# Performance work log

Measured on AMD Instinct MI355X. Metric: run time of the kernel, lower is better.

Reference implementation:

```python
import jax, jax.numpy as jnp
import numpy as np

B, S, H = 8, 1024, 1024
NH, HD = 16, 64
LN_EPS = 1e-12


def setup_inputs() -> dict:
    key = jax.random.key(0)
    ks = jax.random.split(key, 8)
    sd = 0.02
    return {
        "hidden_states": jax.random.normal(ks[0], (B, S, H), jnp.float32),
        "attention_mask": jnp.zeros((B, 1, 1, S), jnp.float32),
        "Wq": jax.random.normal(ks[1], (H, H), jnp.float32) * sd,
        "bq": jnp.zeros((H,), jnp.float32),
        "Wk": jax.random.normal(ks[2], (H, H), jnp.float32) * sd,
        "bk": jnp.zeros((H,), jnp.float32),
        "Wv": jax.random.normal(ks[3], (H, H), jnp.float32) * sd,
        "bv": jnp.zeros((H,), jnp.float32),
        "Wo": jax.random.normal(ks[4], (H, H), jnp.float32) * sd,
        "bo": jnp.zeros((H,), jnp.float32),
        "ln_gamma": jnp.ones((H,), jnp.float32),
        "ln_beta": jnp.zeros((H,), jnp.float32),
    }


def _heads(x):
    # [B,S,H] -> [B,NH,S,HD]
    return x.reshape(B, S, NH, HD).transpose(0, 2, 1, 3)


def reference(hidden_states, attention_mask, Wq, bq, Wk, bk, Wv, bv, Wo, bo, ln_gamma, ln_beta):
    # QKV projections (torch Linear: x @ W.T + b)
    q = _heads(hidden_states @ Wq.T + bq)
    k = _heads(hidden_states @ Wk.T + bk)
    v = _heads(hidden_states @ Wv.T + bv)
    # scaled dot-product attention with additive mask
    scores = jnp.einsum("bhqd,bhkd->bhqk", q, k) / np.sqrt(HD).astype(np.float32)
    scores = scores + attention_mask  # broadcast [B,1,1,S]
    probs = jax.nn.softmax(scores, axis=-1)
    ctx = jnp.einsum("bhqk,bhkd->bhqd", probs, v)
    ctx = ctx.transpose(0, 2, 1, 3).reshape(B, S, H)
    # output projection + residual + LayerNorm
    out = ctx @ Wo.T + bo
    x = out + hidden_states
    mu = jnp.mean(x, axis=-1, keepdims=True)
    var = jnp.var(x, axis=-1, keepdims=True)
    return (x - mu) * jax.lax.rsqrt(var + LN_EPS) * ln_gamma + ln_beta
```

## Files before the change

kernel.cpp:

```cpp
#include <hip/hip_runtime.h>
#include <stdint.h>

typedef __attribute__((ext_vector_type(8))) __bf16 bf16x8;
typedef __attribute__((ext_vector_type(8))) unsigned short ushortx8;
typedef __attribute__((ext_vector_type(4))) unsigned short ushortx4;
typedef __attribute__((ext_vector_type(4))) short short4v;
typedef __attribute__((ext_vector_type(4))) float floatx4;

#define LOG2E 1.4426950408889634f
#define QSCALE 0.18033688011112043f

#define ASYNC16(g, l) __builtin_amdgcn_global_load_lds( \
    (__attribute__((address_space(1))) void*)(g),       \
    (__attribute__((address_space(3))) void*)(l), 16, 0, 0)

__device__ __forceinline__ unsigned short f2bf(float f) {
    unsigned int u = __float_as_uint(f);
    u += 0x7fffu + ((u >> 16) & 1u);
    return (unsigned short)(u >> 16);
}

__device__ __forceinline__ floatx4 mfma32(bf16x8 a, bf16x8 b, floatx4 c) {
    return __builtin_amdgcn_mfma_f32_16x16x32_bf16(a, b, c, 0, 0, 0);
}
__device__ __forceinline__ floatx4 mfma16(short4v a, short4v b, floatx4 c) {
    return __builtin_amdgcn_mfma_f32_16x16x16bf16_1k(a, b, c, 0, 0, 0);
}

__global__ __launch_bounds__(256) void cvt_all(
    const float* __restrict__ hidden,
    const float* __restrict__ Wq, const float* __restrict__ Wk,
    const float* __restrict__ Wv, const float* __restrict__ Wo,
    unsigned short* __restrict__ hid_bf,
    unsigned short* __restrict__ oqkv, unsigned short* __restrict__ oo)
{
    const float* src;
    unsigned short* dst;
    int i;
    if (blockIdx.x < 4096) {
        src = hidden; dst = hid_bf;
        i = blockIdx.x * 256 + threadIdx.x;
    } else {
        int blk = (blockIdx.x - 4096) >> 9;
        src = (blk == 0) ? Wq : (blk == 1) ? Wk : (blk == 2) ? Wv : Wo;
        dst = (blk == 3) ? oo : oqkv + (size_t)blk * 1048576;
        i = ((blockIdx.x - 4096) & 511) * 256 + threadIdx.x;
    }
    const float4* p = (const float4*)src + (size_t)i * 2;
    float4 a = p[0], b = p[1];
    ushortx8 o;
    o[0] = f2bf(a.x); o[1] = f2bf(a.y); o[2] = f2bf(a.z); o[3] = f2bf(a.w);
    o[4] = f2bf(b.x); o[5] = f2bf(b.y); o[6] = f2bf(b.z); o[7] = f2bf(b.w);
    *((ushortx8*)dst + i) = o;
}

template<bool SWAP>
__device__ __forceinline__ void kloop_bk64(
    const unsigned short* __restrict__ Ag,
    const unsigned short* __restrict__ Wg,
    unsigned short* As, unsigned short* Bs,
    int wm, int wn, int l16, int quad, int t,
    floatx4 acc[4][4])
{
#pragma unroll 1
    for (int k0 = 0; k0 < 1024; k0 += 64) {
        __syncthreads();
#pragma unroll
        for (int i = 0; i < 4; i++) {
            ASYNC16(Ag + (size_t)i * 32 * 1024 + k0, As + i * 2048 + t * 8);
            ASYNC16(Wg + (size_t)i * 32 * 1024 + k0, Bs + i * 2048 + t * 8);
        }
        __syncthreads();
#pragma unroll
        for (int s = 0; s < 2; s++) {
            int pb = ((s * 4 + quad) ^ (l16 & 7)) * 8;
            bf16x8 af[4], bfr[4];
#pragma unroll
            for (int mt = 0; mt < 4; mt++)
                af[mt] = *(const bf16x8*)(As + (wm + mt * 16 + l16) * 64 + pb);
#pragma unroll
            for (int nt = 0; nt < 4; nt++)
                bfr[nt] = *(const bf16x8*)(Bs + (wn + nt * 16 + l16) * 64 + pb);
            if (SWAP) {
#pragma unroll
                for (int ft = 0; ft < 4; ft++)
#pragma unroll
                    for (int st = 0; st < 4; st++)
                        acc[ft][st] = mfma32(bfr[ft], af[st], acc[ft][st]);
            } else {
#pragma unroll
                for (int mt = 0; mt < 4; mt++)
#pragma unroll
                    for (int nt = 0; nt < 4; nt++)
                        acc[mt][nt] = mfma32(af[mt], bfr[nt], acc[mt][nt]);
            }
        }
    }
}

__global__ __launch_bounds__(256) void gemm_qkv(
    const unsigned short* __restrict__ A,
    const unsigned short* __restrict__ W,
    const float* __restrict__ bq, const float* __restrict__ bk, const float* __restrict__ bv,
    unsigned short* __restrict__ Qo, unsigned short* __restrict__ Ko,
    unsigned short* __restrict__ Vo)
{
    __shared__ unsigned short As[128 * 64];
    __shared__ unsigned short Bs[128 * 64];
    const int t = threadIdx.x;
    const int wave = t >> 6, lane = t & 63;
    const int quad = lane >> 4, l16 = lane & 15;
    const int wm = (wave >> 1) * 64, wn = (wave & 1) * 64;
    const int srow = t >> 3;
    const int scol = ((t & 7) ^ (srow & 7)) * 8;

    const unsigned short* Ag = A + ((size_t)blockIdx.x * 128 + srow) * 1024 + scol;
    const unsigned short* Wg = W + ((size_t)blockIdx.y * 128 + srow) * 1024 + scol;

    floatx4 acc[4][4] = {};
    kloop_bk64<true>(Ag, Wg, As, Bs, wm, wn, l16, quad, t, acc);

    int y = blockIdx.y;
    if (y < 16) {
        const float* bp = (y < 8) ? bq : bk;
        unsigned short* op = (y < 8) ? Qo : Ko;
        float sc = (y < 8) ? QSCALE : 1.0f;
#pragma unroll
        for (int ft = 0; ft < 4; ft++) {
            int featg = (y * 128 + wn + ft * 16 + quad * 4) & 1023;
            float4 b4 = *(const float4*)(bp + featg);
            int h = featg >> 6, d = featg & 63;
#pragma unroll
            for (int st = 0; st < 4; st++) {
                int sg = blockIdx.x * 128 + wm + st * 16 + l16;
                int b = sg >> 10, s = sg & 1023;
                ushortx4 o4;
                o4[0] = f2bf((acc[ft][st][0] + b4.x) * sc);
                o4[1] = f2bf((acc[ft][st][1] + b4.y) * sc);
                o4[2] = f2bf((acc[ft][st][2] + b4.z) * sc);
                o4[3] = f2bf((acc[ft][st][3] + b4.w) * sc);
                *(ushortx4*)(op + (((size_t)(b * 16 + h) * 1024 + s) * 64 + d)) = o4;
            }
        }
    } else {
#pragma unroll
        for (int ft = 0; ft < 4; ft++) {
            int featg = (y * 128 + wn + ft * 16 + quad * 4) & 1023;
            float4 b4 = *(const float4*)(bv + featg);
#pragma unroll
            for (int r = 0; r < 4; r++) {
                int feat = featg + r;
                int h = feat >> 6, d = feat & 63;
                float bias = (r == 0) ? b4.x : (r == 1) ? b4.y : (r == 2) ? b4.z : b4.w;
#pragma unroll
                for (int st = 0; st < 4; st++) {
                    int sg = blockIdx.x * 128 + wm + st * 16 + l16;
                    int b = sg >> 10, s = sg & 1023;
                    int sp = (s & ~63) + (st >> 1) * 32 + (l16 >> 2) * 8 + (st & 1) * 4 + (l16 & 3);
                    Vo[((size_t)(b * 16 + h) * 64 + d) * 1024 + sp] = f2bf(acc[ft][st][r] + bias);
                }
            }
        }
    }
}

__global__ __launch_bounds__(256) void attn(
    const unsigned short* __restrict__ Q,
    const unsigned short* __restrict__ Kg,
    const unsigned short* __restrict__ Vt,
    const float* __restrict__ mask,
    unsigned short* __restrict__ ctx)
{
    __shared__ unsigned short Qs[128 * 64];
    __shared__ unsigned short Ks[64 * 64];
    __shared__ unsigned short Vs[64 * 64];
    __shared__ float Msall[1024];

    const int t = threadIdx.x;
    const int wave = t >> 6, lane = t & 63, quad = lane >> 4, l16 = lane & 15;
    const int s7 = l16 & 7;
    const int head = blockIdx.y;
    const int b = head >> 4, h = head & 15;
    const int q0 = blockIdx.x * 128;
    const unsigned short* Qh = Q + (size_t)head * 65536;
    const unsigned short* Kh = Kg + (size_t)head * 65536;
    const unsigned short* Vh = Vt + (size_t)head * 65536;

    const int srow = t >> 3;
    const int scol = ((t & 7) ^ (srow & 7)) * 8;

    {
        float4 m4 = *(const float4*)(mask + b * 1024 + t * 4);
        m4.x *= LOG2E; m4.y *= LOG2E; m4.z *= LOG2E; m4.w *= LOG2E;
        *(float4*)(Msall + t * 4) = m4;
    }

#pragma unroll
    for (int i = 0; i < 4; i++)
        ASYNC16(Qh + (size_t)(q0 + i * 32 + srow) * 64 + scol, Qs + i * 2048 + t * 8);
    __syncthreads();

    bf16x8 qf[2][2];
#pragma unroll
    for (int qg = 0; qg < 2; qg++) {
        int qrow = wave * 32 + qg * 16 + l16;
#pragma unroll
        for (int s = 0; s < 2; s++)
            qf[qg][s] = *(const bf16x8*)(Qs + qrow * 64 + (((s * 4 + quad) ^ s7) * 8));
    }

    const short4v ones = {(short)0x3F80, (short)0x3F80, (short)0x3F80, (short)0x3F80};
    floatx4 acc_l[2] = {};
    floatx4 o_acc[2][4] = {};

    for (int k0 = 0; k0 < 1024; k0 += 64) {
        __syncthreads();
#pragma unroll
        for (int i = 0; i < 2; i++) {
            ASYNC16(Kh + (size_t)(k0 + i * 32 + srow) * 64 + scol, Ks + i * 2048 + t * 8);
            ASYNC16(Vh + (size_t)(i * 32 + srow) * 1024 + k0 + scol, Vs + i * 2048 + t * 8);
        }
        __syncthreads();

        bf16x8 kf[4][2];
        floatx4 mk[4];
#pragma unroll
        for (int nt = 0; nt < 4; nt++) {
            int krow = nt * 16 + l16;
#pragma unroll
            for (int s = 0; s < 2; s++)
                kf[nt][s] = *(const bf16x8*)(Ks + krow * 64 + (((s * 4 + quad) ^ s7) * 8));
            mk[nt] = *(const floatx4*)(Msall + k0 + nt * 16 + quad * 4);
        }

        short4v pf[2][4];
#pragma unroll
        for (int qg = 0; qg < 2; qg++) {
#pragma unroll
            for (int nt = 0; nt < 4; nt++) {
                floatx4 z = {0.f, 0.f, 0.f, 0.f};
                z = mfma32(kf[nt][0], qf[qg][0], z);
                z = mfma32(kf[nt][1], qf[qg][1], z);
#pragma unroll
                for (int r = 0; r < 4; r++) {
                    float p = exp2f(z[r] + mk[nt][r]);
                    pf[qg][nt][r] = (short)(__float_as_uint(p) >> 16);
                }
            }
        }

#pragma unroll
        for (int nt = 0; nt < 4; nt++) {
            acc_l[0] = mfma16(ones, pf[0][nt], acc_l[0]);
            acc_l[1] = mfma16(ones, pf[1][nt], acc_l[1]);
        }

#pragma unroll
        for (int dt = 0; dt < 4; dt++) {
            int vrow = dt * 16 + l16;
            ushortx8 v01 = *(const ushortx8*)(Vs + vrow * 64 + ((quad ^ s7) * 8));
            ushortx8 v23 = *(const ushortx8*)(Vs + vrow * 64 + (((quad + 4) ^ s7) * 8));
            short4v vf0 = {(short)v01[0], (short)v01[1], (short)v01[2], (short)v01[3]};
            short4v vf1 = {(short)v01[4], (short)v01[5], (short)v01[6], (short)v01[7]};
            short4v vf2 = {(short)v23[0], (short)v23[1], (short)v23[2], (short)v23[3]};
            short4v vf3 = {(short)v23[4], (short)v23[5], (short)v23[6], (short)v23[7]};
#pragma unroll
            for (int qg = 0; qg < 2; qg++) {
                o_acc[qg][dt] = mfma16(vf0, pf[qg][0], o_acc[qg][dt]);
                o_acc[qg][dt] = mfma16(vf1, pf[qg][1], o_acc[qg][dt]);
                o_acc[qg][dt] = mfma16(vf2, pf[qg][2], o_acc[qg][dt]);
                o_acc[qg][dt] = mfma16(vf3, pf[qg][3], o_acc[qg][dt]);
            }
        }
    }

#pragma unroll
    for (int qg = 0; qg < 2; qg++) {
        float inv_l = 1.0f / acc_l[qg][0];
        int qg_row = q0 + wave * 32 + qg * 16 + l16;
#pragma unroll
        for (int dt = 0; dt < 4; dt++) {
            ushortx4 o4;
#pragma unroll
            for (int r = 0; r < 4; r++) o4[r] = f2bf(o_acc[qg][dt][r] * inv_l);
            *(ushortx4*)(ctx + ((size_t)(b * 1024 + qg_row)) * 1024 + h * 64 + dt * 16 + quad * 4) = o4;
        }
    }
}

__global__ __launch_bounds__(256) void gemm_proj(
    const unsigned short* __restrict__ A,
    const unsigned short* __restrict__ W,
    const float* __restrict__ bo,
    const float* __restrict__ resid,
    float* __restrict__ X)
{
    __shared__ unsigned short As[128 * 64];
    __shared__ unsigned short Bs[128 * 64];
    const int t = threadIdx.x;
    const int wave = t >> 6, lane = t & 63;
    const int quad = lane >> 4, l16 = lane & 15;
    const int wm = (wave >> 1) * 64, wn = (wave & 1) * 64;
    const int srow = t >> 3;
    const int scol = ((t & 7) ^ (srow & 7)) * 8;

    const unsigned short* Ag = A + ((size_t)blockIdx.x * 128 + srow) * 1024 + scol;
    const unsigned short* Wg = W + ((size_t)blockIdx.y * 128 + srow) * 1024 + scol;

    floatx4 acc[4][4] = {};
    kloop_bk64<false>(Ag, Wg, As, Bs, wm, wn, l16, quad, t, acc);

#pragma unroll
    for (int nt = 0; nt < 4; nt++) {
        int gn = blockIdx.y * 128 + wn + nt * 16 + l16;
        float bias = bo[gn];
#pragma unroll
        for (int mt = 0; mt < 4; mt++) {
#pragma unroll
            for (int r = 0; r < 4; r++) {
                int gm = blockIdx.x * 128 + wm + mt * 16 + quad * 4 + r;
                size_t off = (size_t)gm * 1024 + gn;
                X[off] = acc[mt][nt][r] + bias + resid[off];
            }
        }
    }
}

__global__ __launch_bounds__(256) void ln_k(const float* __restrict__ X,
                                            const float* __restrict__ g,
                                            const float* __restrict__ be,
                                            float* __restrict__ out)
{
    int row = blockIdx.x;
    int t = threadIdx.x;
    const float* xr = X + (size_t)row * 1024;
    float4 v = *(const float4*)(xr + t * 4);
    float s = v.x + v.y + v.z + v.w;
    float ss = v.x * v.x + v.y * v.y + v.z * v.z + v.w * v.w;
    for (int off = 1; off < 64; off <<= 1) {
        s += __shfl_xor(s, off);
        ss += __shfl_xor(ss, off);
    }
    __shared__ float red[8];
    int wave = t >> 6, lane = t & 63;
    if (lane == 0) { red[wave] = s; red[4 + wave] = ss; }
    __syncthreads();
    s = red[0] + red[1] + red[2] + red[3];
    ss = red[4] + red[5] + red[6] + red[7];
    float mu = s * (1.f / 1024.f);
    float var = ss * (1.f / 1024.f) - mu * mu;
    float inv = rsqrtf(var + 1e-12f);
    float4 gv = *(const float4*)(g + t * 4);
    float4 bv = *(const float4*)(be + t * 4);
    float4 o;
    o.x = (v.x - mu) * inv * gv.x + bv.x;
    o.y = (v.y - mu) * inv * gv.y + bv.y;
    o.z = (v.z - mu) * inv * gv.z + bv.z;
    o.w = (v.w - mu) * inv * gv.w + bv.w;
    *(float4*)(out + (size_t)row * 1024 + t * 4) = o;
}

extern "C" void kernel_launch(void* const* d_in, const int* in_sizes, int n_in,
                              void* d_out, int out_size, void* d_ws, size_t ws_size,
                              hipStream_t stream)
{
    const float* hidden = (const float*)d_in[0];
    const float* mask   = (const float*)d_in[1];
    const float* Wq = (const float*)d_in[2];
    const float* bq = (const float*)d_in[3];
    const float* Wk = (const float*)d_in[4];
    const float* bk = (const float*)d_in[5];
    const float* Wv = (const float*)d_in[6];
    const float* bv = (const float*)d_in[7];
    const float* Wo = (const float*)d_in[8];
    const float* bo = (const float*)d_in[9];
    const float* gamma = (const float*)d_in[10];
    const float* beta  = (const float*)d_in[11];
    float* out = (float*)d_out;

    char* ws = (char*)d_ws;
    unsigned short* hid_bf  = (unsigned short*)(ws + 0);
    unsigned short* wqkv_bf = (unsigned short*)(ws + 16777216);
    unsigned short* wo_bf   = (unsigned short*)(ws + 23068672);
    unsigned short* vt_bf   = (unsigned short*)(ws + 25165824);
    unsigned short* ctx_bf  = (unsigned short*)(ws + 41943040);
    unsigned short* q_bf    = (unsigned short*)(ws + 58720256);
    unsigned short* k_bf    = (unsigned short*)(ws + 75497472);
    float* x_f = (float*)(ws + 58720256);

    cvt_all<<<6144, 256, 0, stream>>>(hidden, Wq, Wk, Wv, Wo, hid_bf, wqkv_bf, wo_bf);

    gemm_qkv<<<dim3(64, 24), 256, 0, stream>>>(hid_bf, wqkv_bf, bq, bk, bv, q_bf, k_bf, vt_bf);
    attn<<<dim3(8, 128), 256, 0, stream>>>(q_bf, k_bf, vt_bf, mask, ctx_bf);
    gemm_proj<<<dim3(64, 8), 256, 0, stream>>>(ctx_bf, wo_bf, bo, hidden, x_f);
    ln_k<<<8192, 256, 0, stream>>>(x_f, gamma, beta, out);
}
```

Baseline: 288.8 us.

## Halve attention query tile and compute row sums with shuffles instead of MFMA

Each attention block now handles 64 query rows (16 per wave) instead of 128, doubling the grid to 2048 blocks. The softmax denominator is summed in fp32 registers and reduced with two cross-lane shuffles, replacing the extra MFMA against a vector of ones. This cuts per-wave register use and MFMA work, likely raising occupancy. The cost is that every K/V tile is loaded twice as often per query row, and the denominator now uses unrounded fp32 probabilities while the numerator still uses truncated bf16 ones.

```diff
diff --git a/kernel.cpp b/kernel.cpp
--- a/kernel.cpp
+++ b/kernel.cpp
@@ -171,7 +171,7 @@
     const float* __restrict__ mask,
     unsigned short* __restrict__ ctx)
 {
-    __shared__ unsigned short Qs[128 * 64];
+    __shared__ unsigned short Qs[64 * 64];
     __shared__ unsigned short Ks[64 * 64];
     __shared__ unsigned short Vs[64 * 64];
     __shared__ float Msall[1024];
@@ -181,7 +181,7 @@
     const int s7 = l16 & 7;
     const int head = blockIdx.y;
     const int b = head >> 4, h = head & 15;
-    const int q0 = blockIdx.x * 128;
+    const int q0 = blockIdx.x * 64;
     const unsigned short* Qh = Q + (size_t)head * 65536;
     const unsigned short* Kh = Kg + (size_t)head * 65536;
     const unsigned short* Vh = Vt + (size_t)head * 65536;
@@ -196,22 +196,16 @@
     }
 
 #pragma unroll
-    for (int i = 0; i < 4; i++)
+    for (int i = 0; i < 2; i++)
         ASYNC16(Qh + (size_t)(q0 + i * 32 + srow) * 64 + scol, Qs + i * 2048 + t * 8);
     __syncthreads();
 
-    bf16x8 qf[2][2];
-#pragma unroll
-    for (int qg = 0; qg < 2; qg++) {
-        int qrow = wave * 32 + qg * 16 + l16;
-#pragma unroll
-        for (int s = 0; s < 2; s++)
-            qf[qg][s] = *(const bf16x8*)(Qs + qrow * 64 + (((s * 4 + quad) ^ s7) * 8));
-    }
-
-    const short4v ones = {(short)0x3F80, (short)0x3F80, (short)0x3F80, (short)0x3F80};
-    floatx4 acc_l[2] = {};
-    floatx4 o_acc[2][4] = {};
+    int qrow = wave * 16 + l16;
+    bf16x8 qf0 = *(const bf16x8*)(Qs + qrow * 64 + ((quad ^ s7) * 8));
+    bf16x8 qf1 = *(const bf16x8*)(Qs + qrow * 64 + (((4 + quad) ^ s7) * 8));
+
+    float rs_acc = 0.f;
+    floatx4 o_acc[4] = {};
 
     for (int k0 = 0; k0 < 1024; k0 += 64) {
         __syncthreads();
@@ -222,69 +216,51 @@
         }
         __syncthreads();
 
-        bf16x8 kf[4][2];
-        floatx4 mk[4];
+        short4v pf[4];
 #pragma unroll
         for (int nt = 0; nt < 4; nt++) {
             int krow = nt * 16 + l16;
-#pragma unroll
-            for (int s = 0; s < 2; s++)
-                kf[nt][s] = *(const bf16x8*)(Ks + krow * 64 + (((s * 4 + quad) ^ s7) * 8));
-            mk[nt] = *(const floatx4*)(Msall + k0 + nt * 16 + quad * 4);
-        }
-
-        short4v pf[2][4];
-#pragma unroll
-        for (int qg = 0; qg < 2; qg++) {
-#pragma unroll
-            for (int nt = 0; nt < 4; nt++) {
-                floatx4 z = {0.f, 0.f, 0.f, 0.f};
-                z = mfma32(kf[nt][0], qf[qg][0], z);
-                z = mfma32(kf[nt][1], qf[qg][1], z);
-#pragma unroll
-                for (int r = 0; r < 4; r++) {
-                    float p = exp2f(z[r] + mk[nt][r]);
-                    pf[qg][nt][r] = (short)(__float_as_uint(p) >> 16);
-                }
-            }
-        }
-
-#pragma unroll
-        for (int nt = 0; nt < 4; nt++) {
-            acc_l[0] = mfma16(ones, pf[0][nt], acc_l[0]);
-            acc_l[1] = mfma16(ones, pf[1][nt], acc_l[1]);
+            bf16x8 kf0 = *(const bf16x8*)(Ks + krow * 64 + ((quad ^ s7) * 8));
+            bf16x8 kf1 = *(const bf16x8*)(Ks + krow * 64 + (((4 + quad) ^ s7) * 8));
+            floatx4 z = {0.f, 0.f, 0.f, 0.f};
+            z = mfma32(kf0, qf0, z);
+            z = mfma32(kf1, qf1, z);
+            floatx4 mk = *(const floatx4*)(Msall + k0 + nt * 16 + quad * 4);
+#pragma unroll
+            for (int r = 0; r < 4; r++) {
+                float p = exp2f(z[r] + mk[r]);
+                rs_acc += p;
+                pf[nt][r] = (short)(__float_as_uint(p) >> 16);
+            }
         }
 
 #pragma unroll
         for (int dt = 0; dt < 4; dt++) {
             int vrow = dt * 16 + l16;
             ushortx8 v01 = *(const ushortx8*)(Vs + vrow * 64 + ((quad ^ s7) * 8));
-            ushortx8 v23 = *(const ushortx8*)(Vs + vrow * 64 + (((quad + 4) ^ s7) * 8));
+            ushortx8 v23 = *(const ushortx8*)(Vs + vrow * 64 + (((4 + quad) ^ s7) * 8));
             short4v vf0 = {(short)v01[0], (short)v01[1], (short)v01[2], (short)v01[3]};
             short4v vf1 = {(short)v01[4], (short)v01[5], (short)v01[6], (short)v01[7]};
             short4v vf2 = {(short)v23[0], (short)v23[1], (short)v23[2], (short)v23[3]};
             short4v vf3 = {(short)v23[4], (short)v23[5], (short)v23[6], (short)v23[7]};
-#pragma unroll
-            for (int qg = 0; qg < 2; qg++) {
-                o_acc[qg][dt] = mfma16(vf0, pf[qg][0], o_acc[qg][dt]);
-                o_acc[qg][dt] = mfma16(vf1, pf[qg][1], o_acc[qg][dt]);
-                o_acc[qg][dt] = mfma16(vf2, pf[qg][2], o_acc[qg][dt]);
-                o_acc[qg][dt] = mfma16(vf3, pf[qg][3], o_acc[qg][dt]);
-            }
-        }
-    }
-
-#pragma unroll
-    for (int qg = 0; qg < 2; qg++) {
-        float inv_l = 1.0f / acc_l[qg][0];
-        int qg_row = q0 + wave * 32 + qg * 16 + l16;
-#pragma unroll
-        for (int dt = 0; dt < 4; dt++) {
-            ushortx4 o4;
-#pragma unroll
-            for (int r = 0; r < 4; r++) o4[r] = f2bf(o_acc[qg][dt][r] * inv_l);
-            *(ushortx4*)(ctx + ((size_t)(b * 1024 + qg_row)) * 1024 + h * 64 + dt * 16 + quad * 4) = o4;
-        }
+            o_acc[dt] = mfma16(vf0, pf[0], o_acc[dt]);
+            o_acc[dt] = mfma16(vf1, pf[1], o_acc[dt]);
+            o_acc[dt] = mfma16(vf2, pf[2], o_acc[dt]);
+            o_acc[dt] = mfma16(vf3, pf[3], o_acc[dt]);
+        }
+    }
+
+    rs_acc += __shfl_xor(rs_acc, 16);
+    rs_acc += __shfl_xor(rs_acc, 32);
+    float inv_l = 1.0f / rs_acc;
+
+    int qg = q0 + wave * 16 + l16;
+#pragma unroll
+    for (int dt = 0; dt < 4; dt++) {
+        ushortx4 o4;
+#pragma unroll
+        for (int r = 0; r < 4; r++) o4[r] = f2bf(o_acc[dt][r] * inv_l);
+        *(ushortx4*)(ctx + ((size_t)(b * 1024 + qg)) * 1024 + h * 64 + dt * 16 + quad * 4) = o4;
     }
 }
 
@@ -391,7 +367,7 @@
     cvt_all<<<6144, 256, 0, stream>>>(hidden, Wq, Wk, Wv, Wo, hid_bf, wqkv_bf, wo_bf);
 
     gemm_qkv<<<dim3(64, 24), 256, 0, stream>>>(hid_bf, wqkv_bf, bq, bk, bv, q_bf, k_bf, vt_bf);
-    attn<<<dim3(8, 128), 256, 0, stream>>>(q_bf, k_bf, vt_bf, mask, ctx_bf);
+    attn<<<dim3(16, 128), 256, 0, stream>>>(q_bf, k_bf, vt_bf, mask, ctx_bf);
     gemm_proj<<<dim3(64, 8), 256, 0, stream>>>(ctx_bf, wo_bf, bo, hidden, x_f);
     ln_k<<<8192, 256, 0, stream>>>(x_f, gamma, beta, out);
 }
```

Result: faster. 280.8 us (-2.8%).
